# Optimization experiments

Measured on AMD Instinct MI355X. Metric: run time of the kernel, lower is better.

Reference implementation:

```python
import jax, jax.numpy as jnp
import numpy as np

B, C = 1, 1
D = H = W = 128          # volume depth/height/width (z, y, x)
V = U = 128              # detector rows (v) / cols (u)
A = 96                   # projection angles
N_STEPS = 128            # Joseph ray-marching steps
SX = SY = SD = 1.0       # voxel size (sd, sy, sx)
SU = SV = 1.0            # detector spacing (sv, su)


def setup_inputs() -> dict:
    key = jax.random.key(0)
    # model-facing volume [B, C, X, Y, Z]
    vol = jax.random.normal(key, (B, C, W, H, D), dtype=jnp.float32)
    angles = jnp.linspace(0.0, np.pi, A, endpoint=False).astype(jnp.float32)
    return {"vol": vol, "angles": angles}


def _corner(idx, size):
    """Floor/ceil corner indices + zero-padded linear weights (align_corners=True,
    padding_mode='zeros' semantics of F.grid_sample)."""
    i0f = jnp.floor(idx)
    frac = idx - i0f
    i0 = i0f.astype(jnp.int32)
    i1 = i0 + 1
    w0 = jnp.where((i0 >= 0) & (i0 < size), 1.0 - frac, 0.0)
    w1 = jnp.where((i1 >= 0) & (i1 < size), frac, 0.0)
    return jnp.clip(i0, 0, size - 1), jnp.clip(i1, 0, size - 1), w0, w1


def reference(vol, angles):
    # [B,C,X,Y,Z] -> [B,C,D,H,W] (z,y,x ordering used internally)
    v_zyx = jnp.transpose(vol, (0, 1, 4, 3, 2))
    cos_t = jnp.cos(angles)[:, None]   # [A,1]
    sin_t = jnp.sin(angles)[:, None]   # [A,1]
    u = (jnp.arange(U, dtype=jnp.float32) - (U - 1) / 2.0) * SU   # [U]
    v = (jnp.arange(V, dtype=jnp.float32) - (V - 1) / 2.0) * SV   # [V]
    # half ray length = half in-plane diagonal
    T = 0.5 * float(np.sqrt(((W - 1) * SX) ** 2 + ((H - 1) * SY) ** 2))
    delta_t = 2.0 * T / float(N_STEPS)

    x_base = -u[None, :] * sin_t   # [A,U] ray point at t=0
    y_base = u[None, :] * cos_t    # [A,U]
    # z depends only on detector row v; constant along the ray
    z_idx = v / SD + (D - 1) / 2.0                     # [V]
    z0, z1, wz0, wz1 = _corner(z_idx, D)
    z0, z1 = z0[:, None], z1[:, None]                  # [V,1]
    wz0, wz1 = wz0[:, None], wz1[:, None]

    t_vals = -T + (jnp.arange(N_STEPS, dtype=jnp.float32) + 0.5) * delta_t

    def step(acc, t):
        x_idx = (x_base + t * cos_t) / SX + (W - 1) / 2.0   # [A,U]
        y_idx = (y_base + t * sin_t) / SY + (H - 1) / 2.0   # [A,U]
        x0, x1, wx0, wx1 = [a[:, None, :] for a in _corner(x_idx, W)]  # [A,1,U]
        y0, y1, wy0, wy1 = [a[:, None, :] for a in _corner(y_idx, H)]  # [A,1,U]
        g = lambda zi, yi, xi: v_zyx[:, :, zi, yi, xi]      # -> [B,C,A,V,U]
        s = (wz0 * (wy0 * (wx0 * g(z0, y0, x0) + wx1 * g(z0, y0, x1))
                    + wy1 * (wx0 * g(z0, y1, x0) + wx1 * g(z0, y1, x1)))
             + wz1 * (wy0 * (wx0 * g(z1, y0, x0) + wx1 * g(z1, y0, x1))
                      + wy1 * (wx0 * g(z1, y1, x0) + wx1 * g(z1, y1, x1))))
        return acc + s, None

    acc0 = jnp.zeros((B, C, A, V, U), dtype=vol.dtype)
    acc, _ = jax.lax.scan(jax.checkpoint(step), acc0, t_vals)
    sino = acc * jnp.float32(delta_t)            # [B,C,A,V,U]
    # model-facing sinogram [B,C,X=U,A,Z=V]
    return jnp.transpose(sino, (0, 1, 4, 2, 3))
```

## Files before the change

### kernel.cpp

```cpp
#include <hip/hip_runtime.h>
#include <hip/hip_fp16.h>

namespace {
constexpr int A_N = 96;
constexpr int U_N = 128;
constexpr int V_N = 128;
constexpr int W_N = 128;
constexpr int H_N = 128;
constexpr int NSTEPS = 128;
constexpr float T_HALF = 89.80256121069154f;
constexpr float DT = 1.4031650189170554f;
constexpr float INV_DT = 1.0f / DT;
constexpr int PAD = 6;
constexpr int WP = W_N + 2 * PAD;
constexpr int ROW_BYTES = WP * 256;
constexpr int RAYS_PER_BLOCK = 8;
constexpr int BLOCK_THREADS = RAYS_PER_BLOCK * 16;
constexpr int SEGS = 2;
constexpr size_t VOLP_COLS = (size_t)WP * WP;
constexpr size_t VOLP_BYTES = VOLP_COLS * 256;
constexpr size_t SINO = (size_t)U_N * A_N * V_N;
}

__device__ __forceinline__ unsigned int packh2(float a, float b) {
    return (unsigned int)__half_as_ushort(__float2half_rn(a)) |
           ((unsigned int)__half_as_ushort(__float2half_rn(b)) << 16);
}

__global__ __launch_bounds__(256) void vol_pad_f16(
    const float* __restrict__ vol, unsigned int* __restrict__ volp)
{
    const int idx = blockIdx.x * 256 + threadIdx.x;
    if (idx >= (int)(VOLP_COLS * 16)) return;
    const int zo  = idx & 15;
    const int col = idx >> 4;
    const int yp = col % WP;
    const int xp = col / WP;
    const int x = xp - PAD;
    const int y = yp - PAD;
    uint4 o = make_uint4(0u, 0u, 0u, 0u);
    if ((unsigned)x < 128u && (unsigned)y < 128u) {
        const float* src = vol + (((size_t)x * 128 + y) << 7) + zo * 8;
        const float4 f0 = *(const float4*)(src);
        const float4 f1 = *(const float4*)(src + 4);
        o.x = packh2(f0.x, f0.y);
        o.y = packh2(f0.z, f0.w);
        o.z = packh2(f1.x, f1.y);
        o.w = packh2(f1.z, f1.w);
    }
    *(uint4*)((char*)volp + (size_t)col * 256 + zo * 16) = o;
}

__device__ __forceinline__ const char* step_base(
    const char* volc, int lane16, float i_f, float cv, float sv, float xb, float yb,
    float& fx, float& fy)
{
    const float tf = fmaf(i_f + 0.5f, DT, -T_HALF);
    const float xi = fmaf(tf, cv, xb);
    const float yi = fmaf(tf, sv, yb);
    const float fx0 = floorf(xi);
    const float fy0 = floorf(yi);
    fx = xi - fx0;
    fy = yi - fy0;
    const int x0 = (int)fx0;
    const int y0 = (int)fy0;
    const int base = (((x0 + PAD) * WP + (y0 + PAD)) << 8) + lane16;
    return volc + base;
}

__device__ __forceinline__ void consume(
    const uint4& q00, const uint4& q01, const uint4& q10, const uint4& q11,
    float fx, float fy, float* accf)
{
    const float wx0 = 1.f - fx;
    const float wy0 = 1.f - fy;
    const __half2 w00 = __float2half2_rn(wx0 * wy0);
    const __half2 w01 = __float2half2_rn(wx0 * fy);
    const __half2 w10 = __float2half2_rn(fx  * wy0);
    const __half2 w11 = __float2half2_rn(fx  * fy);
    const __half2* h00 = (const __half2*)&q00;
    const __half2* h01 = (const __half2*)&q01;
    const __half2* h10 = (const __half2*)&q10;
    const __half2* h11 = (const __half2*)&q11;
#pragma unroll
    for (int j = 0; j < 4; ++j) {
        __half2 p = __hmul2(w00, h00[j]);
        p = __hfma2(w01, h01[j], p);
        p = __hfma2(w10, h10[j], p);
        p = __hfma2(w11, h11[j], p);
        const float2 f = __half22float2(p);
        accf[2 * j]     += f.x;
        accf[2 * j + 1] += f.y;
    }
}

__global__ __launch_bounds__(BLOCK_THREADS) void joseph_fwd_inc(
    const unsigned short* __restrict__ volp,
    const float* __restrict__ angles,
    float* __restrict__ dst, float scale)
{
    const int zo  = threadIdx.x & 15;
    const int r   = threadIdx.x >> 4;
    const int u_i = blockIdx.x * RAYS_PER_BLOCK + r;
    const int a   = blockIdx.y;

    const int spseg = NSTEPS / gridDim.z;
    const int i0 = blockIdx.z * spseg;
    const int i1 = i0 + spseg;

    const float ang = angles[a];
    const float cv = cosf(ang);
    const float sv = sinf(ang);
    const float up = (float)u_i - 63.5f;
    const float xb = fmaf(-up, sv, 63.5f);
    const float yb = fmaf( up, cv, 63.5f);

    float tlo = -2.f * T_HALF, thi = 2.f * T_HALF;
    if (fabsf(cv) > 1e-6f) {
        const float ta = (-1.f - xb) / cv, tb = (128.f - xb) / cv;
        tlo = fmaxf(tlo, fminf(ta, tb));
        thi = fminf(thi, fmaxf(ta, tb));
    } else if (xb <= -1.f || xb >= 128.f) { thi = tlo - 1.f; }
    if (fabsf(sv) > 1e-6f) {
        const float ta = (-1.f - yb) / sv, tb = (128.f - yb) / sv;
        tlo = fmaxf(tlo, fminf(ta, tb));
        thi = fminf(thi, fmaxf(ta, tb));
    } else if (yb <= -1.f || yb >= 128.f) { thi = tlo - 1.f; }
    const int ilo = (int)floorf(fmaf(tlo + T_HALF, INV_DT, -0.5f)) - 1;
    const int ihi = (int)ceilf (fmaf(thi + T_HALF, INV_DT, -0.5f)) + 1;
    int lo = min(max(ilo, i0), i1);
    int hi = min(max(ihi + 1, i0), i1);
    lo &= ~1;
    hi = (hi + 1) & ~1;

    const char* __restrict__ volc = (const char*)volp;
    const int lane16 = zo << 4;

    float accf[8];
#pragma unroll
    for (int k = 0; k < 8; ++k) accf[k] = 0.f;

    for (int i = lo; i < hi; i += 2) {
        float fxA, fyA, fxB, fyB;
        const char* pA = step_base(volc, lane16, (float)i,       cv, sv, xb, yb, fxA, fyA);
        const char* pB = step_base(volc, lane16, (float)(i + 1), cv, sv, xb, yb, fxB, fyB);

        const uint4 qA00 = *(const uint4*)(pA);
        const uint4 qA01 = *(const uint4*)(pA + 256);
        const uint4 qA10 = *(const uint4*)(pA + ROW_BYTES);
        const uint4 qA11 = *(const uint4*)(pA + ROW_BYTES + 256);
        const uint4 qB00 = *(const uint4*)(pB);
        const uint4 qB01 = *(const uint4*)(pB + 256);
        const uint4 qB10 = *(const uint4*)(pB + ROW_BYTES);
        const uint4 qB11 = *(const uint4*)(pB + ROW_BYTES + 256);

        consume(qA00, qA01, qA10, qA11, fxA, fyA, accf);
        consume(qB00, qB01, qB10, qB11, fxB, fyB, accf);
    }

    float* op = dst + (size_t)blockIdx.z * SINO + ((size_t)u_i * A_N + a) * V_N + 8 * zo;
    *(float4*)(op)     = make_float4(accf[0] * scale, accf[1] * scale, accf[2] * scale, accf[3] * scale);
    *(float4*)(op + 4) = make_float4(accf[4] * scale, accf[5] * scale, accf[6] * scale, accf[7] * scale);
}

__global__ __launch_bounds__(256) void reduce_segs2(
    const float4* __restrict__ p, float4* __restrict__ out)
{
    const size_t i = (size_t)blockIdx.x * 256 + threadIdx.x;
    const size_t q = SINO / 4;
    const float4 a = p[i];
    const float4 b = p[i + q];
    out[i] = make_float4((a.x + b.x) * DT, (a.y + b.y) * DT,
                         (a.z + b.z) * DT, (a.w + b.w) * DT);
}

__global__ __launch_bounds__(256) void joseph_fwd_f32(
    const float* __restrict__ vol,
    const float* __restrict__ angles,
    float* __restrict__ out)
{
    const int zo  = threadIdx.x & 15;
    const int r   = threadIdx.x >> 4;
    const int u_i = blockIdx.x * 16 + r;
    const int a   = blockIdx.y;

    const float ang = angles[a];
    const float c = cosf(ang);
    const float s = sinf(ang);
    const float u = (float)u_i - 63.5f;
    const float xb = fmaf(-u, s, 63.5f);
    const float yb = fmaf( u, c, 63.5f);

    const float* volz = vol + 8 * zo;
    float4 accA = make_float4(0.f, 0.f, 0.f, 0.f);
    float4 accB = make_float4(0.f, 0.f, 0.f, 0.f);

    for (int i = 0; i < NSTEPS; ++i) {
        const float t  = fmaf((float)i + 0.5f, DT, -T_HALF);
        const float xi = fmaf(t, c, xb);
        const float yi = fmaf(t, s, yb);
        const float fx0f = floorf(xi);
        const float fy0f = floorf(yi);
        const int x0 = (int)fx0f;
        const int y0 = (int)fy0f;
        const float fx = xi - fx0f;
        const float fy = yi - fy0f;
        const int x1 = x0 + 1;
        const int y1 = y0 + 1;
        const float wx0 = (x0 >= 0 && x0 < W_N) ? (1.f - fx) : 0.f;
        const float wx1 = (x1 >= 0 && x1 < W_N) ? fx : 0.f;
        const float wy0 = (y0 >= 0 && y0 < H_N) ? (1.f - fy) : 0.f;
        const float wy1 = (y1 >= 0 && y1 < H_N) ? fy : 0.f;
        if ((wx0 + wx1) == 0.f || (wy0 + wy1) == 0.f) continue;
        const int cx0 = min(max(x0, 0), W_N - 1);
        const int cx1 = min(max(x1, 0), W_N - 1);
        const int cy0 = min(max(y0, 0), H_N - 1);
        const int cy1 = min(max(y1, 0), H_N - 1);
        const float* p00 = volz + ((cx0 * H_N + cy0) << 7);
        const float* p01 = volz + ((cx1 * H_N + cy0) << 7);
        const float* p10 = volz + ((cx0 * H_N + cy1) << 7);
        const float* p11 = volz + ((cx1 * H_N + cy1) << 7);
        const float4 v00a = *(const float4*)(p00);
        const float4 v00b = *(const float4*)(p00 + 4);
        const float4 v01a = *(const float4*)(p01);
        const float4 v01b = *(const float4*)(p01 + 4);
        const float4 v10a = *(const float4*)(p10);
        const float4 v10b = *(const float4*)(p10 + 4);
        const float4 v11a = *(const float4*)(p11);
        const float4 v11b = *(const float4*)(p11 + 4);
        const float w00 = wx0 * wy0, w01 = wx1 * wy0, w10 = wx0 * wy1, w11 = wx1 * wy1;
        accA.x = fmaf(w00, v00a.x, fmaf(w01, v01a.x, fmaf(w10, v10a.x, fmaf(w11, v11a.x, accA.x))));
        accA.y = fmaf(w00, v00a.y, fmaf(w01, v01a.y, fmaf(w10, v10a.y, fmaf(w11, v11a.y, accA.y))));
        accA.z = fmaf(w00, v00a.z, fmaf(w01, v01a.z, fmaf(w10, v10a.z, fmaf(w11, v11a.z, accA.z))));
        accA.w = fmaf(w00, v00a.w, fmaf(w01, v01a.w, fmaf(w10, v10a.w, fmaf(w11, v11a.w, accA.w))));
        accB.x = fmaf(w00, v00b.x, fmaf(w01, v01b.x, fmaf(w10, v10b.x, fmaf(w11, v11b.x, accB.x))));
        accB.y = fmaf(w00, v00b.y, fmaf(w01, v01b.y, fmaf(w10, v10b.y, fmaf(w11, v11b.y, accB.y))));
        accB.z = fmaf(w00, v00b.z, fmaf(w01, v01b.z, fmaf(w10, v10b.z, fmaf(w11, v11b.z, accB.z))));
        accB.w = fmaf(w00, v00b.w, fmaf(w01, v01b.w, fmaf(w10, v10b.w, fmaf(w11, v11b.w, accB.w))));
    }

    float* op = out + ((size_t)u_i * A_N + a) * V_N + 8 * zo;
    *(float4*)(op)     = make_float4(accA.x * DT, accA.y * DT, accA.z * DT, accA.w * DT);
    *(float4*)(op + 4) = make_float4(accB.x * DT, accB.y * DT, accB.z * DT, accB.w * DT);
}

extern "C" void kernel_launch(void* const* d_in, const int* in_sizes, int n_in,
                              void* d_out, int out_size, void* d_ws, size_t ws_size,
                              hipStream_t stream) {
    const float* vol    = (const float*)d_in[0];
    const float* angles = (const float*)d_in[1];
    float* out          = (float*)d_out;

    const size_t need_full = VOLP_BYTES + SEGS * SINO * sizeof(float);
    const int pad_blocks = (int)((VOLP_COLS * 16 + 255) / 256);

    if (ws_size >= VOLP_BYTES) {
        unsigned int* volp = (unsigned int*)d_ws;
        hipLaunchKernelGGL(vol_pad_f16, dim3(pad_blocks), dim3(256), 0, stream, vol, volp);
        if (ws_size >= need_full) {
            float* partial = (float*)((char*)d_ws + VOLP_BYTES);
            dim3 grid(U_N / RAYS_PER_BLOCK, A_N, SEGS);
            hipLaunchKernelGGL(joseph_fwd_inc, grid, dim3(BLOCK_THREADS), 0, stream,
                               (const unsigned short*)volp, angles, partial, 1.0f);
            hipLaunchKernelGGL(reduce_segs2, dim3(SINO / 4 / 256), dim3(256), 0, stream,
                               (const float4*)partial, (float4*)out);
        } else {
            dim3 grid(U_N / RAYS_PER_BLOCK, A_N, 1);
            hipLaunchKernelGGL(joseph_fwd_inc, grid, dim3(BLOCK_THREADS), 0, stream,
                               (const unsigned short*)volp, angles, out, DT);
        }
    } else {
        dim3 grid(U_N / 16, A_N);
        hipLaunchKernelGGL(joseph_fwd_f32, grid, dim3(256), 0, stream, vol, angles, out);
    }
}
```

Before: 111.3 us.

## Spread bilinear corners across wave lanes and drop split-step reduction pass

Each ray is now handled by a full 64-lane wave, where four 16-lane groups each load one bilinear corner. Each group accumulates its weighted samples in fp16 and flushes them to fp32 every four steps. The four corner partials are combined with cross-lane shuffles before writing. This replaces the two-segment step split, its partial buffer and the separate reduce kernel, with the aim of cutting per-thread load count and an extra launch and memory pass. The cost is four times more threads per ray, idle lanes during the store, and more fp16 rounding from accumulating several steps in half precision.

```diff
diff --git a/kernel.cpp b/kernel.cpp
--- a/kernel.cpp
+++ b/kernel.cpp
@@ -14,13 +14,12 @@
 constexpr int PAD = 6;
 constexpr int WP = W_N + 2 * PAD;
 constexpr int ROW_BYTES = WP * 256;
-constexpr int RAYS_PER_BLOCK = 8;
-constexpr int BLOCK_THREADS = RAYS_PER_BLOCK * 16;
-constexpr int SEGS = 2;
 constexpr size_t VOLP_COLS = (size_t)WP * WP;
 constexpr size_t VOLP_BYTES = VOLP_COLS * 256;
 constexpr size_t SINO = (size_t)U_N * A_N * V_N;
 }
+
+typedef __attribute__((ext_vector_type(4))) unsigned int u32x4;
 
 __device__ __forceinline__ unsigned int packh2(float a, float b) {
     return (unsigned int)__half_as_ushort(__float2half_rn(a)) |
@@ -51,62 +50,23 @@
     *(uint4*)((char*)volp + (size_t)col * 256 + zo * 16) = o;
 }
 
-__device__ __forceinline__ const char* step_base(
-    const char* volc, int lane16, float i_f, float cv, float sv, float xb, float yb,
-    float& fx, float& fy)
-{
-    const float tf = fmaf(i_f + 0.5f, DT, -T_HALF);
-    const float xi = fmaf(tf, cv, xb);
-    const float yi = fmaf(tf, sv, yb);
-    const float fx0 = floorf(xi);
-    const float fy0 = floorf(yi);
-    fx = xi - fx0;
-    fy = yi - fy0;
-    const int x0 = (int)fx0;
-    const int y0 = (int)fy0;
-    const int base = (((x0 + PAD) * WP + (y0 + PAD)) << 8) + lane16;
-    return volc + base;
-}
-
-__device__ __forceinline__ void consume(
-    const uint4& q00, const uint4& q01, const uint4& q10, const uint4& q11,
-    float fx, float fy, float* accf)
-{
-    const float wx0 = 1.f - fx;
-    const float wy0 = 1.f - fy;
-    const __half2 w00 = __float2half2_rn(wx0 * wy0);
-    const __half2 w01 = __float2half2_rn(wx0 * fy);
-    const __half2 w10 = __float2half2_rn(fx  * wy0);
-    const __half2 w11 = __float2half2_rn(fx  * fy);
-    const __half2* h00 = (const __half2*)&q00;
-    const __half2* h01 = (const __half2*)&q01;
-    const __half2* h10 = (const __half2*)&q10;
-    const __half2* h11 = (const __half2*)&q11;
-#pragma unroll
-    for (int j = 0; j < 4; ++j) {
-        __half2 p = __hmul2(w00, h00[j]);
-        p = __hfma2(w01, h01[j], p);
-        p = __hfma2(w10, h10[j], p);
-        p = __hfma2(w11, h11[j], p);
-        const float2 f = __half22float2(p);
-        accf[2 * j]     += f.x;
-        accf[2 * j + 1] += f.y;
-    }
-}
-
-__global__ __launch_bounds__(BLOCK_THREADS) void joseph_fwd_inc(
+__global__ __launch_bounds__(256) void joseph_fwd_wave(
     const unsigned short* __restrict__ volp,
     const float* __restrict__ angles,
-    float* __restrict__ dst, float scale)
+    float* __restrict__ out)
 {
-    const int zo  = threadIdx.x & 15;
-    const int r   = threadIdx.x >> 4;
-    const int u_i = blockIdx.x * RAYS_PER_BLOCK + r;
-    const int a   = blockIdx.y;
-
-    const int spseg = NSTEPS / gridDim.z;
-    const int i0 = blockIdx.z * spseg;
-    const int i1 = i0 + spseg;
+    const int lane = threadIdx.x & 63;
+    const int wv   = threadIdx.x >> 6;
+    const int u_i  = blockIdx.x * 4 + wv;
+    const int a    = blockIdx.y;
+
+    const int c = lane >> 4;
+    const int k = lane & 15;
+    const int laneOff = ((c & 1) << 8) + ((c >> 1) * ROW_BYTES) + (k << 4);
+    const float sxw = (c >> 1) ? 1.f : -1.f;
+    const float bxw = (c >> 1) ? 0.f : 1.f;
+    const float syw = (c & 1) ? 1.f : -1.f;
+    const float byw = (c & 1) ? 0.f : 1.f;
 
     const float ang = angles[a];
     const float cv = cosf(ang);
@@ -128,50 +88,69 @@
     } else if (yb <= -1.f || yb >= 128.f) { thi = tlo - 1.f; }
     const int ilo = (int)floorf(fmaf(tlo + T_HALF, INV_DT, -0.5f)) - 1;
     const int ihi = (int)ceilf (fmaf(thi + T_HALF, INV_DT, -0.5f)) + 1;
-    int lo = min(max(ilo, i0), i1);
-    int hi = min(max(ihi + 1, i0), i1);
-    lo &= ~1;
-    hi = (hi + 1) & ~1;
+    const int lo = min(max(ilo, 0), NSTEPS);
+    const int hi = min(max(ihi + 1, 0), NSTEPS);
 
     const char* __restrict__ volc = (const char*)volp;
-    const int lane16 = zo << 4;
-
+
+    __half2 hacc[4];
     float accf[8];
 #pragma unroll
-    for (int k = 0; k < 8; ++k) accf[k] = 0.f;
-
-    for (int i = lo; i < hi; i += 2) {
-        float fxA, fyA, fxB, fyB;
-        const char* pA = step_base(volc, lane16, (float)i,       cv, sv, xb, yb, fxA, fyA);
-        const char* pB = step_base(volc, lane16, (float)(i + 1), cv, sv, xb, yb, fxB, fyB);
-
-        const uint4 qA00 = *(const uint4*)(pA);
-        const uint4 qA01 = *(const uint4*)(pA + 256);
-        const uint4 qA10 = *(const uint4*)(pA + ROW_BYTES);
-        const uint4 qA11 = *(const uint4*)(pA + ROW_BYTES + 256);
-        const uint4 qB00 = *(const uint4*)(pB);
-        const uint4 qB01 = *(const uint4*)(pB + 256);
-        const uint4 qB10 = *(const uint4*)(pB + ROW_BYTES);
-        const uint4 qB11 = *(const uint4*)(pB + ROW_BYTES + 256);
-
-        consume(qA00, qA01, qA10, qA11, fxA, fyA, accf);
-        consume(qB00, qB01, qB10, qB11, fxB, fyB, accf);
-    }
-
-    float* op = dst + (size_t)blockIdx.z * SINO + ((size_t)u_i * A_N + a) * V_N + 8 * zo;
-    *(float4*)(op)     = make_float4(accf[0] * scale, accf[1] * scale, accf[2] * scale, accf[3] * scale);
-    *(float4*)(op + 4) = make_float4(accf[4] * scale, accf[5] * scale, accf[6] * scale, accf[7] * scale);
-}
-
-__global__ __launch_bounds__(256) void reduce_segs2(
-    const float4* __restrict__ p, float4* __restrict__ out)
-{
-    const size_t i = (size_t)blockIdx.x * 256 + threadIdx.x;
-    const size_t q = SINO / 4;
-    const float4 a = p[i];
-    const float4 b = p[i + q];
-    out[i] = make_float4((a.x + b.x) * DT, (a.y + b.y) * DT,
-                         (a.z + b.z) * DT, (a.w + b.w) * DT);
+    for (int j = 0; j < 4; ++j) hacc[j] = __float2half2_rn(0.f);
+#pragma unroll
+    for (int j = 0; j < 8; ++j) accf[j] = 0.f;
+
+    int kc = 0;
+    for (int i = lo; i < hi; ++i) {
+        const float tf = fmaf((float)i + 0.5f, DT, -T_HALF);
+        const float xi = fmaf(tf, cv, xb);
+        const float yi = fmaf(tf, sv, yb);
+        const float fx0 = floorf(xi);
+        const float fy0 = floorf(yi);
+        const float fx = xi - fx0;
+        const float fy = yi - fy0;
+        const int x0 = (int)fx0;
+        const int y0 = (int)fy0;
+        const int off = (((x0 + PAD) * WP + (y0 + PAD)) << 8) + laneOff;
+
+        const u32x4 q = *(const u32x4*)(volc + off);
+
+        const float w = fmaf(sxw, fx, bxw) * fmaf(syw, fy, byw);
+        const __half2 wh = __float2half2_rn(w);
+        hacc[0] = __hfma2(wh, __builtin_bit_cast(__half2, (unsigned int)q[0]), hacc[0]);
+        hacc[1] = __hfma2(wh, __builtin_bit_cast(__half2, (unsigned int)q[1]), hacc[1]);
+        hacc[2] = __hfma2(wh, __builtin_bit_cast(__half2, (unsigned int)q[2]), hacc[2]);
+        hacc[3] = __hfma2(wh, __builtin_bit_cast(__half2, (unsigned int)q[3]), hacc[3]);
+
+        if (((++kc) & 3) == 0) {
+#pragma unroll
+            for (int j = 0; j < 4; ++j) {
+                const float2 f = __half22float2(hacc[j]);
+                accf[2 * j]     += f.x;
+                accf[2 * j + 1] += f.y;
+                hacc[j] = __float2half2_rn(0.f);
+            }
+        }
+    }
+#pragma unroll
+    for (int j = 0; j < 4; ++j) {
+        const float2 f = __half22float2(hacc[j]);
+        accf[2 * j]     += f.x;
+        accf[2 * j + 1] += f.y;
+    }
+
+#pragma unroll
+    for (int j = 0; j < 8; ++j) {
+        accf[j] += __shfl_xor(accf[j], 16);
+        accf[j] += __shfl_xor(accf[j], 32);
+    }
+
+    float* op = out + ((size_t)u_i * A_N + a) * V_N + 8 * k;
+    if (c == 0) {
+        *(float4*)(op) = make_float4(accf[0] * DT, accf[1] * DT, accf[2] * DT, accf[3] * DT);
+    } else if (c == 1) {
+        *(float4*)(op + 4) = make_float4(accf[4] * DT, accf[5] * DT, accf[6] * DT, accf[7] * DT);
+    }
 }
 
 __global__ __launch_bounds__(256) void joseph_fwd_f32(
@@ -251,24 +230,14 @@
     const float* angles = (const float*)d_in[1];
     float* out          = (float*)d_out;
 
-    const size_t need_full = VOLP_BYTES + SEGS * SINO * sizeof(float);
     const int pad_blocks = (int)((VOLP_COLS * 16 + 255) / 256);
 
     if (ws_size >= VOLP_BYTES) {
         unsigned int* volp = (unsigned int*)d_ws;
         hipLaunchKernelGGL(vol_pad_f16, dim3(pad_blocks), dim3(256), 0, stream, vol, volp);
-        if (ws_size >= need_full) {
-            float* partial = (float*)((char*)d_ws + VOLP_BYTES);
-            dim3 grid(U_N / RAYS_PER_BLOCK, A_N, SEGS);
-            hipLaunchKernelGGL(joseph_fwd_inc, grid, dim3(BLOCK_THREADS), 0, stream,
-                               (const unsigned short*)volp, angles, partial, 1.0f);
-            hipLaunchKernelGGL(reduce_segs2, dim3(SINO / 4 / 256), dim3(256), 0, stream,
-                               (const float4*)partial, (float4*)out);
-        } else {
-            dim3 grid(U_N / RAYS_PER_BLOCK, A_N, 1);
-            hipLaunchKernelGGL(joseph_fwd_inc, grid, dim3(BLOCK_THREADS), 0, stream,
-                               (const unsigned short*)volp, angles, out, DT);
-        }
+        dim3 grid(U_N / 4, A_N);
+        hipLaunchKernelGGL(joseph_fwd_wave, grid, dim3(256), 0, stream,
+                           (const unsigned short*)volp, angles, out);
     } else {
         dim3 grid(U_N / 16, A_N);
         hipLaunchKernelGGL(joseph_fwd_f32, grid, dim3(256), 0, stream, vol, angles, out);
```

Result: slower. 140.6 us (+26.3%).
